# Kernel tuning notes

Measured on AMD Instinct MI355X. Metric: run time of the kernel, lower is better.

The kernel has to match this reference:

```python
import jax, jax.numpy as jnp
import numpy as np

HIDDEN = 2048
N_HEADS = 16
N_KV_HEADS = 4
HEAD_DIM = HIDDEN // N_HEADS  # 128
ROPE_THETA = 10000.0
BATCH = 2
SEQ = 2048


def setup_inputs() -> dict:
    key = jax.random.key(0)
    k1, k2, k3, k4, k5 = jax.random.split(key, 5)
    s = 0.02
    return {
        "hidden_states": jax.random.normal(k1, (BATCH, SEQ, HIDDEN), dtype=jnp.float32),
        "attention_mask": jnp.zeros((BATCH, 1, 1, SEQ), dtype=jnp.float32),
        "Wq": jax.random.normal(k2, (HIDDEN, N_HEADS * HEAD_DIM), dtype=jnp.float32) * s,
        "Wk": jax.random.normal(k3, (HIDDEN, N_KV_HEADS * HEAD_DIM), dtype=jnp.float32) * s,
        "Wv": jax.random.normal(k4, (HIDDEN, N_KV_HEADS * HEAD_DIM), dtype=jnp.float32) * s,
        "Wo": jax.random.normal(k5, (N_HEADS * HEAD_DIM, HIDDEN), dtype=jnp.float32) * s,
    }


def _rope_cos_sin(seq_len, dtype):
    inv_freq = 1.0 / (ROPE_THETA ** (jnp.arange(0, HEAD_DIM, 2, dtype=jnp.float32) / HEAD_DIM))
    t = jnp.arange(seq_len, dtype=jnp.float32)
    freqs = t[:, None] * inv_freq[None, :]            # [S, D/2]
    emb = jnp.concatenate([freqs, freqs], axis=-1)    # [S, D]
    cos = jnp.cos(emb)[None, None, :, :].astype(dtype)  # [1,1,S,D]
    sin = jnp.sin(emb)[None, None, :, :].astype(dtype)
    return cos, sin


def _apply_rope(x, cos, sin):
    # x: [B,H,S,D]; faithful to torch code: rotated = cat((-x[...,1::2], x[...,::2]), -1)
    x1 = x[..., ::2]
    x2 = x[..., 1::2]
    rotated = jnp.concatenate([-x2, x1], axis=-1)
    return x * cos + rotated * sin


def reference(hidden_states, attention_mask, Wq, Wk, Wv, Wo):
    B, S, _ = hidden_states.shape
    scale = HEAD_DIM ** -0.5

    q = (hidden_states @ Wq).reshape(B, S, N_HEADS, HEAD_DIM).transpose(0, 2, 1, 3)      # [B,H,S,D]
    k = (hidden_states @ Wk).reshape(B, S, N_KV_HEADS, HEAD_DIM).transpose(0, 2, 1, 3)   # [B,KV,S,D]
    v = (hidden_states @ Wv).reshape(B, S, N_KV_HEADS, HEAD_DIM).transpose(0, 2, 1, 3)

    cos, sin = _rope_cos_sin(S, hidden_states.dtype)
    q = _apply_rope(q, cos, sin)
    k = _apply_rope(k, cos, sin)

    rep = N_HEADS // N_KV_HEADS
    k = jnp.repeat(k, rep, axis=1)  # [B,H,S,D]
    v = jnp.repeat(v, rep, axis=1)

    scores = jnp.einsum("bhqd,bhkd->bhqk", q, k) * scale  # [B,H,S,S]
    causal = jnp.tril(jnp.ones((S, S), dtype=bool))[None, None]
    scores = jnp.where(causal, scores, -jnp.inf)
    scores = scores + attention_mask  # additive float mask, broadcast [B,1,1,S]

    attn = jax.nn.softmax(scores, axis=-1)
    out = jnp.einsum("bhqk,bhkd->bhqd", attn, v)           # [B,H,S,D]
    out = out.transpose(0, 2, 1, 3).reshape(B, S, N_HEADS * HEAD_DIM)
    return out @ Wo
```

## Files before the change

kernel.cpp:

```cpp
#include <hip/hip_runtime.h>
#include <hip/hip_bf16.h>

#define BATCH 2
#define SEQ   2048
#define NH    16
#define NKV   4
#define HD    128
#define KDIM  2048
#define MROWS 4096
#define NQKV  3072

typedef __attribute__((ext_vector_type(8))) short  s16x8;
typedef __attribute__((ext_vector_type(4))) short  s16x4;
typedef __attribute__((ext_vector_type(4))) float  f32x4;
typedef __attribute__((ext_vector_type(8))) __bf16 b16x8;

#define BARRIER_LDS() do { \
    asm volatile("s_waitcnt lgkmcnt(0)" ::: "memory"); \
    __builtin_amdgcn_s_barrier(); \
  } while (0)

__device__ __forceinline__ unsigned short f2bf(float f) {
  __hip_bfloat16 h = __float2bfloat16(f);
  return *reinterpret_cast<unsigned short*>(&h);
}
__device__ __forceinline__ float bf2f(unsigned short h) {
  union { unsigned int u; float f; } x; x.u = ((unsigned int)h) << 16;
  return x.f;
}

__device__ __forceinline__ f32x4 MFMA16(s16x8 a, s16x8 b, f32x4 c) {
  return __builtin_amdgcn_mfma_f32_16x16x32_bf16(
      __builtin_bit_cast(b16x8, a), __builtin_bit_cast(b16x8, b), c, 0, 0, 0);
}

__device__ __forceinline__ void gload_lds16(const void* g, void* lds) {
  __builtin_amdgcn_global_load_lds(
      (const __attribute__((address_space(1))) void*)g,
      (__attribute__((address_space(3))) void*)lds, 16, 0, 0);
}

__global__ __launch_bounds__(256) void transpose_convert(
    const float* __restrict__ W, unsigned short* __restrict__ WT, int Kd, int Nd) {
  __shared__ float tile[32][33];
  int n0 = blockIdx.x * 32, k0 = blockIdx.y * 32;
  int tx = threadIdx.x & 31, ty = threadIdx.x >> 5;
#pragma unroll
  for (int i = 0; i < 4; ++i)
    tile[ty + i * 8][tx] = W[(size_t)(k0 + ty + i * 8) * Nd + n0 + tx];
  __syncthreads();
#pragma unroll
  for (int i = 0; i < 4; ++i)
    WT[(size_t)(n0 + ty + i * 8) * Kd + k0 + tx] = f2bf(tile[tx][ty + i * 8]);
}

__global__ __launch_bounds__(256) void conv_bf16(
    const float* __restrict__ X, unsigned short* __restrict__ Y) {
  int i = blockIdx.x * 256 + threadIdx.x;
  const float4 a = ((const float4*)X)[2 * i];
  const float4 b = ((const float4*)X)[2 * i + 1];
  s16x8 o;
  o[0] = (short)f2bf(a.x); o[1] = (short)f2bf(a.y);
  o[2] = (short)f2bf(a.z); o[3] = (short)f2bf(a.w);
  o[4] = (short)f2bf(b.x); o[5] = (short)f2bf(b.y);
  o[6] = (short)f2bf(b.z); o[7] = (short)f2bf(b.w);
  ((s16x8*)Y)[i] = o;
}

__global__ __launch_bounds__(256) void rope_table_kernel(float* __restrict__ tbl) {
  int i = blockIdx.x * 256 + threadIdx.x;
  int s = i >> 6, j = i & 63;
  float inv = powf(10000.0f, -(float)(2 * j) * (1.0f / 128.0f));
  float f = (float)s * inv;
  tbl[2 * i]     = cosf(f);
  tbl[2 * i + 1] = sinf(f);
}

__global__ __launch_bounds__(256) void gemm_qkv(
    const unsigned short* __restrict__ A, const unsigned short* __restrict__ BT,
    unsigned short* __restrict__ Qo, unsigned short* __restrict__ Ko,
    unsigned short* __restrict__ Vo) {
  __shared__ __align__(16) unsigned short la[128][32];
  __shared__ __align__(16) unsigned short lb[128][32];
  int tid = threadIdx.x, lane = tid & 63, w = tid >> 6;
  int lin = blockIdx.x;
  int swz = (lin & 7) * 96 + (lin >> 3);
  int bx = swz % 24, by = swz / 24;
  int m0 = by * 128, n0 = bx * 128;
  int wr = (w >> 1) * 64, wc = (w & 1) * 64;
  int fr = lane & 15, kg = (lane >> 4) * 8, rg = (lane >> 4) * 4;
  f32x4 acc[4][4] = {};
  for (int kt = 0; kt < KDIM; kt += 32) {
    __syncthreads();
#pragma unroll
    for (int i = 0; i < 2; ++i) {
      int idx = tid + i * 256;
      int row = idx >> 2, seg = idx & 3;
      gload_lds16(A + (size_t)(m0 + row) * KDIM + kt + seg * 8,
                  (char*)la + (size_t)(i * 256 + w * 64) * 16);
      gload_lds16(BT + (size_t)(n0 + row) * KDIM + kt + seg * 8,
                  (char*)lb + (size_t)(i * 256 + w * 64) * 16);
    }
    __syncthreads();
    s16x8 af[4], bf[4];
#pragma unroll
    for (int mi = 0; mi < 4; ++mi) af[mi] = *(const s16x8*)(&la[wr + mi * 16 + fr][kg]);
#pragma unroll
    for (int ni = 0; ni < 4; ++ni) bf[ni] = *(const s16x8*)(&lb[wc + ni * 16 + fr][kg]);
#pragma unroll
    for (int mi = 0; mi < 4; ++mi)
#pragma unroll
      for (int ni = 0; ni < 4; ++ni) acc[mi][ni] = MFMA16(af[mi], bf[ni], acc[mi][ni]);
  }
  int rbase = m0 + wr + rg;
#pragma unroll
  for (int ni = 0; ni < 4; ++ni) {
    int gn = n0 + wc + ni * 16 + fr;
    if (gn < 2048) {
      int hh = gn >> 7, d = gn & 127;
#pragma unroll
      for (int mi = 0; mi < 4; ++mi)
#pragma unroll
        for (int r = 0; r < 4; ++r) {
          int grow = rbase + mi * 16 + r;
          int bb = grow >> 11, ss = grow & 2047;
          Qo[((size_t)(bb * NH + hh) * SEQ + ss) * HD + d] = f2bf(acc[mi][ni][r]);
        }
    } else if (gn < 2560) {
      int c = gn - 2048, kvh = c >> 7, d = c & 127;
#pragma unroll
      for (int mi = 0; mi < 4; ++mi)
#pragma unroll
        for (int r = 0; r < 4; ++r) {
          int grow = rbase + mi * 16 + r;
          int bb = grow >> 11, ss = grow & 2047;
          Ko[((size_t)(bb * NKV + kvh) * SEQ + ss) * HD + d] = f2bf(acc[mi][ni][r]);
        }
    } else {
      int c = gn - 2560, kvh = c >> 7, d = c & 127;
#pragma unroll
      for (int mi = 0; mi < 4; ++mi) {
        int grow0 = rbase + mi * 16;
        int bb = grow0 >> 11, ss = grow0 & 2047;
        s16x4 pk;
#pragma unroll
        for (int r = 0; r < 4; ++r) pk[r] = (short)f2bf(acc[mi][ni][r]);
        *(s16x4*)(Vo + ((size_t)(bb * NKV + kvh) * HD + d) * SEQ + ss) = pk;
      }
    }
  }
}

__global__ __launch_bounds__(256) void gemm_out(
    const unsigned short* __restrict__ A, const unsigned short* __restrict__ BT,
    float* __restrict__ C) {
  __shared__ __align__(16) unsigned short la[128][32];
  __shared__ __align__(16) unsigned short lb[128][32];
  int tid = threadIdx.x, lane = tid & 63, w = tid >> 6;
  int lin = blockIdx.x;
  int swz = (lin & 7) * 64 + (lin >> 3);
  int bx = swz % 16, by = swz / 16;
  int m0 = by * 128, n0 = bx * 128;
  int wr = (w >> 1) * 64, wc = (w & 1) * 64;
  int fr = lane & 15, kg = (lane >> 4) * 8, rg = (lane >> 4) * 4;
  f32x4 acc[4][4] = {};
  for (int kt = 0; kt < KDIM; kt += 32) {
    __syncthreads();
#pragma unroll
    for (int i = 0; i < 2; ++i) {
      int idx = tid + i * 256;
      int row = idx >> 2, seg = idx & 3;
      gload_lds16(A + (size_t)(m0 + row) * KDIM + kt + seg * 8,
                  (char*)la + (size_t)(i * 256 + w * 64) * 16);
      gload_lds16(BT + (size_t)(n0 + row) * KDIM + kt + seg * 8,
                  (char*)lb + (size_t)(i * 256 + w * 64) * 16);
    }
    __syncthreads();
    s16x8 af[4], bf[4];
#pragma unroll
    for (int mi = 0; mi < 4; ++mi) af[mi] = *(const s16x8*)(&la[wr + mi * 16 + fr][kg]);
#pragma unroll
    for (int ni = 0; ni < 4; ++ni) bf[ni] = *(const s16x8*)(&lb[wc + ni * 16 + fr][kg]);
#pragma unroll
    for (int mi = 0; mi < 4; ++mi)
#pragma unroll
      for (int ni = 0; ni < 4; ++ni) acc[mi][ni] = MFMA16(af[mi], bf[ni], acc[mi][ni]);
  }
  int rbase = m0 + wr + rg;
#pragma unroll
  for (int ni = 0; ni < 4; ++ni) {
    int gn = n0 + wc + ni * 16 + fr;
#pragma unroll
    for (int mi = 0; mi < 4; ++mi)
#pragma unroll
      for (int r = 0; r < 4; ++r)
        C[(size_t)(rbase + mi * 16 + r) * 2048 + gn] = acc[mi][ni][r];
  }
}

__global__ __launch_bounds__(256) void rope2(
    unsigned short* __restrict__ X, const float* __restrict__ tbl) {
  __shared__ __align__(16) unsigned short xs[32][136];
  int tid = threadIdx.x;
  size_t r0 = (size_t)blockIdx.x * 32;
#pragma unroll
  for (int i = 0; i < 2; ++i) {
    int idx = tid + i * 256;
    int pr = idx >> 4, seg = idx & 15;
    *(s16x8*)(&xs[pr][seg * 8]) = *(const s16x8*)(X + (r0 + pr) * 128 + seg * 8);
  }
  __syncthreads();
  int pr = tid >> 3, jb = (tid & 7) * 8;
  size_t row = r0 + pr;
  int s = (int)(row & (SEQ - 1));
  s16x8 o0, o1;
#pragma unroll
  for (int j0 = 0; j0 < 8; ++j0) {
    int j = jb + j0;
    float c  = tbl[(s * 64 + j) * 2];
    float sn = tbl[(s * 64 + j) * 2 + 1];
    float xj   = bf2f(xs[pr][j]);
    float xj64 = bf2f(xs[pr][j + 64]);
    float x2j  = bf2f(xs[pr][2 * j]);
    float x2j1 = bf2f(xs[pr][2 * j + 1]);
    o0[j0] = (short)f2bf(xj * c - x2j1 * sn);
    o1[j0] = (short)f2bf(xj64 * c + x2j * sn);
  }
  unsigned short* xp = X + row * 128;
  *(s16x8*)(xp + jb)      = o0;
  *(s16x8*)(xp + 64 + jb) = o1;
}

__global__ __launch_bounds__(512, 2) void attn_fwd(
    const unsigned short* __restrict__ Q, const unsigned short* __restrict__ K,
    const unsigned short* __restrict__ VT, const float* __restrict__ mask,
    unsigned short* __restrict__ O) {
  __shared__ __align__(16) unsigned short kt_[2][64][136];
  __shared__ __align__(16) unsigned short vt_[128][68];
  __shared__ __align__(16) unsigned short pt_[8][16][36];

  int tid = threadIdx.x, lane = tid & 63, w = tid >> 6;
  int l = blockIdx.x;
  int grp = l & 7, slot = l >> 3;
  int hloc = slot & 3, p = slot >> 2;
  int b = grp >> 2, kvh = grp & 3, h = kvh * 4 + hloc;
  int half = w >> 2, wsub = w & 3;
  int qt = half ? p : 31 - p;
  int qw = qt * 64 + wsub * 16;
  int fr = lane & 15, g = lane >> 4, kg = g * 8, rg = g * 4;

  const unsigned short* Qb = Q + (size_t)(b * NH + h) * SEQ * HD;
  const unsigned short* Kb = K + (size_t)(b * NKV + kvh) * SEQ * HD;
  const unsigned short* Vb = VT + (size_t)(b * NKV + kvh) * HD * SEQ;
  const float* mb = mask + (size_t)b * SEQ;

  int krow = tid >> 4, kpos = (tid & 15) * 8;
  int vrow = tid >> 3, vcol = (tid & 7) * 8;

  const float sc2 = 0.12751744584812722f;
  const float L2E = 1.44269504088896f;
  int bS = b * SEQ;
  int ntiles = 32 - p;

  s16x8 aq[4];
#pragma unroll
  for (int dc = 0; dc < 4; ++dc)
    aq[dc] = *(const s16x8*)(Qb + (size_t)(qw + fr) * HD + dc * 32 + kg);

  f32x4 oacc[8] = {};
  float m_r = -3e38f, l_r = 0.f;

  s16x8 kreg[2], vreg[2];
  kreg[0] = *(const s16x8*)(Kb + (size_t)krow * HD + kpos);
  kreg[1] = *(const s16x8*)(Kb + (size_t)(krow + 32) * HD + kpos);
  vreg[0] = *(const s16x8*)(Vb + (size_t)vrow * SEQ + vcol);
  vreg[1] = *(const s16x8*)(Vb + (size_t)(vrow + 64) * SEQ + vcol);
  *(s16x8*)(&kt_[0][krow][kpos])      = kreg[0];
  *(s16x8*)(&kt_[0][krow + 32][kpos]) = kreg[1];
  BARRIER_LDS();

  int cur = 0;
  for (int t = 0; t < ntiles; ++t) {
    int kv0 = t * 64;
    bool notlast = (t + 1 < ntiles);
    bool active = (kv0 <= qw + 15);
    bool diag   = (kv0 + 63 > qw);

    *(s16x8*)(&vt_[vrow][vcol])      = vreg[0];
    *(s16x8*)(&vt_[vrow + 64][vcol]) = vreg[1];
    if (notlast) {
      kreg[0] = *(const s16x8*)(Kb + (size_t)(kv0 + 64 + krow) * HD + kpos);
      kreg[1] = *(const s16x8*)(Kb + (size_t)(kv0 + 96 + krow) * HD + kpos);
    }

    f32x4 sf[4];
    if (active) {
      __builtin_amdgcn_s_setprio(1);
#pragma unroll
      for (int mk = 0; mk < 4; ++mk) {
        s16x8 ak[4];
#pragma unroll
        for (int dc = 0; dc < 4; ++dc)
          ak[dc] = *(const s16x8*)(&kt_[cur][mk * 16 + fr][dc * 32 + kg]);
        sf[mk] = f32x4{0.f, 0.f, 0.f, 0.f};
#pragma unroll
        for (int dc = 0; dc < 4; ++dc)
          sf[mk] = MFMA16(ak[dc], aq[dc], sf[mk]);
      }
      __builtin_amdgcn_s_setprio(0);

#pragma unroll
      for (int mk = 0; mk < 4; ++mk) {
        float4 mv = *(const float4*)(mb + kv0 + mk * 16 + rg);
        float mvr[4] = {mv.x * L2E, mv.y * L2E, mv.z * L2E, mv.w * L2E};
        if (diag) {
#pragma unroll
          for (int r = 0; r < 4; ++r) {
            int kv = kv0 + mk * 16 + rg + r;
            float v = sf[mk][r] * sc2 + mvr[r];
            sf[mk][r] = (kv <= qw + fr) ? v : -3e38f;
          }
        } else {
#pragma unroll
          for (int r = 0; r < 4; ++r)
            sf[mk][r] = sf[mk][r] * sc2 + mvr[r];
        }
      }

      float pm01a = fmaxf(sf[0][0], sf[0][1]), pm01b = fmaxf(sf[0][2], sf[0][3]);
      float pm11a = fmaxf(sf[1][0], sf[1][1]), pm11b = fmaxf(sf[1][2], sf[1][3]);
      float pm21a = fmaxf(sf[2][0], sf[2][1]), pm21b = fmaxf(sf[2][2], sf[2][3]);
      float pm31a = fmaxf(sf[3][0], sf[3][1]), pm31b = fmaxf(sf[3][2], sf[3][3]);
      float pm0 = fmaxf(pm01a, pm01b), pm1 = fmaxf(pm11a, pm11b);
      float pm2 = fmaxf(pm21a, pm21b), pm3 = fmaxf(pm31a, pm31b);
      float pm = fmaxf(fmaxf(pm0, pm1), fmaxf(pm2, pm3));
      pm = fmaxf(pm, __shfl_xor(pm, 16, 64));
      pm = fmaxf(pm, __shfl_xor(pm, 32, 64));
      if (!__all(pm - m_r <= 8.0f)) {
        float mo = m_r;
        float mn = fmaxf(mo, pm);
        float al = exp2f(mo - mn);
        m_r = mn;
        l_r *= al;
#pragma unroll
        for (int r = 0; r < 4; ++r) {
          float ar = __shfl(al, rg + r, 16);
#pragma unroll
          for (int od = 0; od < 8; ++od) oacc[od][r] *= ar;
        }
      }
      float rs = 0.f;
#pragma unroll
      for (int mk = 0; mk < 4; ++mk)
#pragma unroll
        for (int r = 0; r < 4; ++r) {
          float ppv = exp2f(sf[mk][r] - m_r);
          sf[mk][r] = ppv;
          rs += ppv;
        }
      rs += __shfl_xor(rs, 16, 64);
      rs += __shfl_xor(rs, 32, 64);
      l_r += rs;
    }

    if (notlast) {
      *(s16x8*)(&kt_[cur ^ 1][krow][kpos])      = kreg[0];
      *(s16x8*)(&kt_[cur ^ 1][krow + 32][kpos]) = kreg[1];
    }
    BARRIER_LDS();

    if (notlast) {
      vreg[0] = *(const s16x8*)(Vb + (size_t)vrow * SEQ + kv0 + 64 + vcol);
      vreg[1] = *(const s16x8*)(Vb + (size_t)(vrow + 64) * SEQ + kv0 + 64 + vcol);
    }

    if (active) {
#pragma unroll
      for (int kk = 0; kk < 2; ++kk) {
#pragma unroll
        for (int mh = 0; mh < 2; ++mh) {
          int mk = kk * 2 + mh;
          s16x4 pk;
#pragma unroll
          for (int r = 0; r < 4; ++r) pk[r] = (short)f2bf(sf[mk][r]);
          *(s16x4*)(&pt_[w][fr][mh * 16 + rg]) = pk;
        }
        s16x8 ap = *(const s16x8*)(&pt_[w][fr][kg]);
        __builtin_amdgcn_s_setprio(1);
#pragma unroll
        for (int od = 0; od < 8; ++od) {
          s16x8 bv = *(const s16x8*)(&vt_[od * 16 + fr][kk * 32 + kg]);
          oacc[od] = MFMA16(ap, bv, oacc[od]);
        }
        __builtin_amdgcn_s_setprio(0);
      }
    }
    BARRIER_LDS();
    cur ^= 1;
  }

  float iv = 1.0f / l_r;
  float ivr[4];
#pragma unroll
  for (int r = 0; r < 4; ++r) ivr[r] = __shfl(iv, rg + r, 16);
#pragma unroll
  for (int r = 0; r < 4; ++r) {
    unsigned short* op = O + (size_t)(bS + qw + rg + r) * 2048 + h * 128 + fr;
#pragma unroll
    for (int od = 0; od < 8; ++od)
      op[od * 16] = f2bf(oacc[od][r] * ivr[r]);
  }
}

extern "C" void kernel_launch(void* const* d_in, const int* in_sizes, int n_in,
                              void* d_out, int out_size, void* d_ws, size_t ws_size,
                              hipStream_t stream) {
  const float* hidden = (const float*)d_in[0];
  const float* mask   = (const float*)d_in[1];
  const float* Wq     = (const float*)d_in[2];
  const float* Wk     = (const float*)d_in[3];
  const float* Wv     = (const float*)d_in[4];
  const float* Wo     = (const float*)d_in[5];
  float* out = (float*)d_out;

  char* ws = (char*)d_ws;
  unsigned short* BT  = (unsigned short*)(ws);
  unsigned short* WoT = (unsigned short*)(ws + 12582912);
  unsigned short* Qb  = (unsigned short*)(ws + 20971520);
  unsigned short* Kb  = (unsigned short*)(ws + 37748736);
  unsigned short* VT  = (unsigned short*)(ws + 41943040);
  unsigned short* AO  = (unsigned short*)(ws + 46137344);
  float*          tbl = (float*)(ws + 62914560);
  unsigned short* Ab  = AO;

  conv_bf16<<<MROWS * KDIM / (256 * 8), 256, 0, stream>>>(hidden, Ab);
  transpose_convert<<<dim3(64, 64), 256, 0, stream>>>(Wq, BT, KDIM, 2048);
  transpose_convert<<<dim3(16, 64), 256, 0, stream>>>(Wk, BT + (size_t)2048 * KDIM, KDIM, 512);
  transpose_convert<<<dim3(16, 64), 256, 0, stream>>>(Wv, BT + (size_t)2560 * KDIM, KDIM, 512);
  transpose_convert<<<dim3(64, 64), 256, 0, stream>>>(Wo, WoT, KDIM, 2048);
  rope_table_kernel<<<512, 256, 0, stream>>>(tbl);

  gemm_qkv<<<dim3(768), 256, 0, stream>>>(Ab, BT, Qb, Kb, VT);
  rope2<<<(BATCH * NH * SEQ) / 32, 256, 0, stream>>>(Qb, tbl);
  rope2<<<(BATCH * NKV * SEQ) / 32, 256, 0, stream>>>(Kb, tbl);
  attn_fwd<<<dim3(512), 512, 0, stream>>>(Qb, Kb, VT, mask, AO);
  gemm_out<<<dim3(512), 256, 0, stream>>>(AO, WoT, out);
}
```

Baseline: 230.9 us.

## Widen GEMM K-tile with XOR-swizzled LDS and stream V from global in attention

```diff
diff --git a/kernel.cpp b/kernel.cpp
--- a/kernel.cpp
+++ b/kernel.cpp
@@ -80,37 +80,47 @@
     const unsigned short* __restrict__ A, const unsigned short* __restrict__ BT,
     unsigned short* __restrict__ Qo, unsigned short* __restrict__ Ko,
     unsigned short* __restrict__ Vo) {
-  __shared__ __align__(16) unsigned short la[128][32];
-  __shared__ __align__(16) unsigned short lb[128][32];
+  __shared__ __align__(16) unsigned short la[128][64];
+  __shared__ __align__(16) unsigned short lb[128][64];
   int tid = threadIdx.x, lane = tid & 63, w = tid >> 6;
   int lin = blockIdx.x;
   int swz = (lin & 7) * 96 + (lin >> 3);
   int bx = swz % 24, by = swz / 24;
   int m0 = by * 128, n0 = bx * 128;
   int wr = (w >> 1) * 64, wc = (w & 1) * 64;
-  int fr = lane & 15, kg = (lane >> 4) * 8, rg = (lane >> 4) * 4;
+  int fr = lane & 15, g = lane >> 4, rg = g * 4;
+  int srow = tid >> 3, sc_ = ((tid & 7) ^ (srow & 7)) * 8;
   f32x4 acc[4][4] = {};
-  for (int kt = 0; kt < KDIM; kt += 32) {
+  for (int kt = 0; kt < KDIM; kt += 64) {
     __syncthreads();
 #pragma unroll
-    for (int i = 0; i < 2; ++i) {
+    for (int i = 0; i < 4; ++i) {
       int idx = tid + i * 256;
-      int row = idx >> 2, seg = idx & 3;
-      gload_lds16(A + (size_t)(m0 + row) * KDIM + kt + seg * 8,
-                  (char*)la + (size_t)(i * 256 + w * 64) * 16);
-      gload_lds16(BT + (size_t)(n0 + row) * KDIM + kt + seg * 8,
-                  (char*)lb + (size_t)(i * 256 + w * 64) * 16);
+      int row = srow + i * 32;
+      gload_lds16(A + (size_t)(m0 + row) * KDIM + kt + sc_,
+                  (char*)la + (size_t)idx * 16);
+      gload_lds16(BT + (size_t)(n0 + row) * KDIM + kt + sc_,
+                  (char*)lb + (size_t)idx * 16);
     }
     __syncthreads();
-    s16x8 af[4], bf[4];
-#pragma unroll
-    for (int mi = 0; mi < 4; ++mi) af[mi] = *(const s16x8*)(&la[wr + mi * 16 + fr][kg]);
-#pragma unroll
-    for (int ni = 0; ni < 4; ++ni) bf[ni] = *(const s16x8*)(&lb[wc + ni * 16 + fr][kg]);
-#pragma unroll
-    for (int mi = 0; mi < 4; ++mi)
-#pragma unroll
-      for (int ni = 0; ni < 4; ++ni) acc[mi][ni] = MFMA16(af[mi], bf[ni], acc[mi][ni]);
+#pragma unroll
+    for (int kk = 0; kk < 2; ++kk) {
+      s16x8 af[4], bf[4];
+#pragma unroll
+      for (int mi = 0; mi < 4; ++mi) {
+        int R = wr + mi * 16 + fr;
+        af[mi] = *(const s16x8*)((const unsigned short*)la + R * 64 + ((((kk << 2) | g)) ^ (R & 7)) * 8);
+      }
+#pragma unroll
+      for (int ni = 0; ni < 4; ++ni) {
+        int R = wc + ni * 16 + fr;
+        bf[ni] = *(const s16x8*)((const unsigned short*)lb + R * 64 + ((((kk << 2) | g)) ^ (R & 7)) * 8);
+      }
+#pragma unroll
+      for (int mi = 0; mi < 4; ++mi)
+#pragma unroll
+        for (int ni = 0; ni < 4; ++ni) acc[mi][ni] = MFMA16(af[mi], bf[ni], acc[mi][ni]);
+    }
   }
   int rbase = m0 + wr + rg;
 #pragma unroll
@@ -154,37 +164,47 @@
 __global__ __launch_bounds__(256) void gemm_out(
     const unsigned short* __restrict__ A, const unsigned short* __restrict__ BT,
     float* __restrict__ C) {
-  __shared__ __align__(16) unsigned short la[128][32];
-  __shared__ __align__(16) unsigned short lb[128][32];
+  __shared__ __align__(16) unsigned short la[128][64];
+  __shared__ __align__(16) unsigned short lb[128][64];
   int tid = threadIdx.x, lane = tid & 63, w = tid >> 6;
   int lin = blockIdx.x;
   int swz = (lin & 7) * 64 + (lin >> 3);
   int bx = swz % 16, by = swz / 16;
   int m0 = by * 128, n0 = bx * 128;
   int wr = (w >> 1) * 64, wc = (w & 1) * 64;
-  int fr = lane & 15, kg = (lane >> 4) * 8, rg = (lane >> 4) * 4;
+  int fr = lane & 15, g = lane >> 4, rg = g * 4;
+  int srow = tid >> 3, sc_ = ((tid & 7) ^ (srow & 7)) * 8;
   f32x4 acc[4][4] = {};
-  for (int kt = 0; kt < KDIM; kt += 32) {
+  for (int kt = 0; kt < KDIM; kt += 64) {
     __syncthreads();
 #pragma unroll
-    for (int i = 0; i < 2; ++i) {
+    for (int i = 0; i < 4; ++i) {
       int idx = tid + i * 256;
-      int row = idx >> 2, seg = idx & 3;
-      gload_lds16(A + (size_t)(m0 + row) * KDIM + kt + seg * 8,
-                  (char*)la + (size_t)(i * 256 + w * 64) * 16);
-      gload_lds16(BT + (size_t)(n0 + row) * KDIM + kt + seg * 8,
-                  (char*)lb + (size_t)(i * 256 + w * 64) * 16);
+      int row = srow + i * 32;
+      gload_lds16(A + (size_t)(m0 + row) * KDIM + kt + sc_,
+                  (char*)la + (size_t)idx * 16);
+      gload_lds16(BT + (size_t)(n0 + row) * KDIM + kt + sc_,
+                  (char*)lb + (size_t)idx * 16);
     }
     __syncthreads();
-    s16x8 af[4], bf[4];
-#pragma unroll
-    for (int mi = 0; mi < 4; ++mi) af[mi] = *(const s16x8*)(&la[wr + mi * 16 + fr][kg]);
-#pragma unroll
-    for (int ni = 0; ni < 4; ++ni) bf[ni] = *(const s16x8*)(&lb[wc + ni * 16 + fr][kg]);
-#pragma unroll
-    for (int mi = 0; mi < 4; ++mi)
-#pragma unroll
-      for (int ni = 0; ni < 4; ++ni) acc[mi][ni] = MFMA16(af[mi], bf[ni], acc[mi][ni]);
+#pragma unroll
+    for (int kk = 0; kk < 2; ++kk) {
+      s16x8 af[4], bf[4];
+#pragma unroll
+      for (int mi = 0; mi < 4; ++mi) {
+        int R = wr + mi * 16 + fr;
+        af[mi] = *(const s16x8*)((const unsigned short*)la + R * 64 + ((((kk << 2) | g)) ^ (R & 7)) * 8);
+      }
+#pragma unroll
+      for (int ni = 0; ni < 4; ++ni) {
+        int R = wc + ni * 16 + fr;
+        bf[ni] = *(const s16x8*)((const unsigned short*)lb + R * 64 + ((((kk << 2) | g)) ^ (R & 7)) * 8);
+      }
+#pragma unroll
+      for (int mi = 0; mi < 4; ++mi)
+#pragma unroll
+        for (int ni = 0; ni < 4; ++ni) acc[mi][ni] = MFMA16(af[mi], bf[ni], acc[mi][ni]);
+    }
   }
   int rbase = m0 + wr + rg;
 #pragma unroll
@@ -236,7 +256,6 @@
     const unsigned short* __restrict__ VT, const float* __restrict__ mask,
     unsigned short* __restrict__ O) {
   __shared__ __align__(16) unsigned short kt_[2][64][136];
-  __shared__ __align__(16) unsigned short vt_[128][68];
   __shared__ __align__(16) unsigned short pt_[8][16][36];
 
   int tid = threadIdx.x, lane = tid & 63, w = tid >> 6;
@@ -255,7 +274,6 @@
   const float* mb = mask + (size_t)b * SEQ;
 
   int krow = tid >> 4, kpos = (tid & 15) * 8;
-  int vrow = tid >> 3, vcol = (tid & 7) * 8;
 
   const float sc2 = 0.12751744584812722f;
   const float L2E = 1.44269504088896f;
@@ -270,11 +288,9 @@
   f32x4 oacc[8] = {};
   float m_r = -3e38f, l_r = 0.f;
 
-  s16x8 kreg[2], vreg[2];
+  s16x8 kreg[2];
   kreg[0] = *(const s16x8*)(Kb + (size_t)krow * HD + kpos);
   kreg[1] = *(const s16x8*)(Kb + (size_t)(krow + 32) * HD + kpos);
-  vreg[0] = *(const s16x8*)(Vb + (size_t)vrow * SEQ + vcol);
-  vreg[1] = *(const s16x8*)(Vb + (size_t)(vrow + 64) * SEQ + vcol);
   *(s16x8*)(&kt_[0][krow][kpos])      = kreg[0];
   *(s16x8*)(&kt_[0][krow + 32][kpos]) = kreg[1];
   BARRIER_LDS();
@@ -286,8 +302,6 @@
     bool active = (kv0 <= qw + 15);
     bool diag   = (kv0 + 63 > qw);
 
-    *(s16x8*)(&vt_[vrow][vcol])      = vreg[0];
-    *(s16x8*)(&vt_[vrow + 64][vcol]) = vreg[1];
     if (notlast) {
       kreg[0] = *(const s16x8*)(Kb + (size_t)(kv0 + 64 + krow) * HD + kpos);
       kreg[1] = *(const s16x8*)(Kb + (size_t)(kv0 + 96 + krow) * HD + kpos);
@@ -367,12 +381,6 @@
       *(s16x8*)(&kt_[cur ^ 1][krow][kpos])      = kreg[0];
       *(s16x8*)(&kt_[cur ^ 1][krow + 32][kpos]) = kreg[1];
     }
-    BARRIER_LDS();
-
-    if (notlast) {
-      vreg[0] = *(const s16x8*)(Vb + (size_t)vrow * SEQ + kv0 + 64 + vcol);
-      vreg[1] = *(const s16x8*)(Vb + (size_t)(vrow + 64) * SEQ + kv0 + 64 + vcol);
-    }
 
     if (active) {
 #pragma unroll
@@ -389,7 +397,7 @@
         __builtin_amdgcn_s_setprio(1);
 #pragma unroll
         for (int od = 0; od < 8; ++od) {
-          s16x8 bv = *(const s16x8*)(&vt_[od * 16 + fr][kk * 32 + kg]);
+          s16x8 bv = *(const s16x8*)(Vb + (size_t)(od * 16 + fr) * SEQ + kv0 + kk * 32 + kg);
           oacc[od] = MFMA16(ap, bv, oacc[od]);
         }
         __builtin_amdgcn_s_setprio(0);
```

After: 381.3 us, median of 2. 65.1% more time.
